# Performance work log

Measured on AMD Instinct MI355X. Metric: run time of the kernel, lower is better.

The kernel has to match this reference:

```python
import jax, jax.numpy as jnp
import numpy as np

ALPHA = 0.25
GAMMA = 2.0
W_CLASS, W_BBOX, W_GIOU, W_EMBED = 1.0, 1.0, 1.0, 0.5
EPS = 1e-8


def box_cxcywh_to_xyxy(b):
    cx, cy, w, h = b[..., 0], b[..., 1], b[..., 2], b[..., 3]
    return jnp.stack([cx - 0.5 * w, cy - 0.5 * h, cx + 0.5 * w, cy + 0.5 * h], axis=-1)


def generalized_box_iou(boxes1, boxes2):
    # boxes1 [N,4], boxes2 [M,4] in xyxy -> [N,M]
    area1 = (boxes1[:, 2] - boxes1[:, 0]) * (boxes1[:, 3] - boxes1[:, 1])
    area2 = (boxes2[:, 2] - boxes2[:, 0]) * (boxes2[:, 3] - boxes2[:, 1])
    lt = jnp.maximum(boxes1[:, None, :2], boxes2[None, :, :2])  # [N,M,2]
    rb = jnp.minimum(boxes1[:, None, 2:], boxes2[None, :, 2:])
    wh = jnp.clip(rb - lt, 0.0)
    inter = wh[..., 0] * wh[..., 1]
    union = area1[:, None] + area2[None, :] - inter
    iou = inter / union
    lt_e = jnp.minimum(boxes1[:, None, :2], boxes2[None, :, :2])
    rb_e = jnp.maximum(boxes1[:, None, 2:], boxes2[None, :, 2:])
    wh_e = jnp.clip(rb_e - lt_e, 0.0)
    area_e = wh_e[..., 0] * wh_e[..., 1]
    return iou - (area_e - union) / area_e


def setup_inputs() -> dict:
    key = jax.random.key(0)
    ks = jax.random.split(key, 6)
    B, Q, C, D, M = 16, 1024, 91, 512, 1600
    pred_logits = jax.random.normal(ks[0], (B, Q, C), dtype=jnp.float32)
    pred_boxes = jax.random.uniform(ks[1], (B, Q, 4), dtype=jnp.float32)
    pred_embed = jax.random.normal(ks[2], (B, Q, D), dtype=jnp.float32)
    text_embeddings = jax.random.normal(ks[3], (C, D), dtype=jnp.float32)
    tgt_ids = jax.random.randint(ks[4], (M,), 0, C, dtype=jnp.int64 if jax.config.jax_enable_x64 else jnp.int32)
    tgt_bbox = jax.random.uniform(ks[5], (M, 4), dtype=jnp.float32)
    return {
        'pred_logits': pred_logits,
        'pred_boxes': pred_boxes,
        'pred_embed': pred_embed,
        'text_embeddings': text_embeddings,
        'tgt_ids': tgt_ids,
        'tgt_bbox': tgt_bbox,
    }


def reference(pred_logits, pred_boxes, pred_embed, text_embeddings, tgt_ids, tgt_bbox):
    B, Q, _ = pred_logits.shape
    N = B * Q
    # --- focal class cost on gathered target-class columns: [N, M]
    logits = pred_logits.reshape(N, -1)
    p = jax.nn.sigmoid(logits[:, tgt_ids])
    pos_cost = ALPHA * (1.0 - p) ** GAMMA * (-jnp.log(p + EPS))
    neg_cost = (1.0 - ALPHA) * p ** GAMMA * (-jnp.log(1.0 - p + EPS))
    cost_class = pos_cost - neg_cost
    # --- L1 box cost (cdist, p=1): [N, M]
    out_bbox = pred_boxes.reshape(N, 4)
    cost_bbox = jnp.sum(jnp.abs(out_bbox[:, None, :] - tgt_bbox[None, :, :]), axis=-1)
    # --- GIoU cost: [N, M]
    cost_giou = -generalized_box_iou(box_cxcywh_to_xyxy(out_bbox), box_cxcywh_to_xyxy(tgt_bbox))
    # --- embedding cosine cost: [N, M]
    v = pred_embed.reshape(N, -1)
    v = v / jnp.linalg.norm(v, axis=1, keepdims=True)
    te = text_embeddings[tgt_ids]  # [M, D]
    cost_embed = 1.0 - v @ te.T
    C = W_BBOX * cost_bbox + W_CLASS * cost_class + W_GIOU * cost_giou + W_EMBED * cost_embed
    return C.reshape(B, Q, -1)
```

## Files before the change

kernel.cpp:

```cpp
#include <hip/hip_runtime.h>
#include <hip/hip_bf16.h>

using bf16x8 = __attribute__((ext_vector_type(8))) short;
using f32x4  = __attribute__((ext_vector_type(4))) float;

__device__ __forceinline__ unsigned short f2bf(float x) {
    unsigned int u = __float_as_uint(x);
    return (unsigned short)((u + 0x7FFFu + ((u >> 16) & 1u)) >> 16);
}

__global__ __launch_bounds__(256)
void k_prep(const float* __restrict__ te, unsigned short* __restrict__ te_bf) {
    const int r = blockIdx.x;
    for (int i = threadIdx.x; i < 512; i += 256) {
        const float v = (r < 91) ? te[(size_t)r * 512 + i] : 0.f;
        te_bf[(size_t)r * 512 + i] = f2bf(v);
    }
}

__global__ __launch_bounds__(256)
void k_class_embed(const float* __restrict__ logits,
                   const float* __restrict__ embed,
                   const unsigned short* __restrict__ te_bf,
                   float* __restrict__ ccombo)
{
    __shared__ float accs[4][16 * 96];
    __shared__ float sq_s[4][16];

    const int tid  = threadIdx.x;
    const int lane = tid & 63;
    const int wv   = tid >> 6;
    const int r16  = lane & 15;
    const int q    = lane >> 4;
    const int n0   = blockIdx.x * 16;

    f32x4 acc[6];
#pragma unroll
    for (int j = 0; j < 6; ++j) acc[j] = (f32x4){0.f, 0.f, 0.f, 0.f};
    float sumsq = 0.f;

    const float* arow = embed + (size_t)(n0 + r16) * 512 + wv * 128 + q * 8;
#pragma unroll
    for (int ks = 0; ks < 4; ++ks) {
        const float4 a0 = *(const float4*)(arow + ks * 32);
        const float4 a1 = *(const float4*)(arow + ks * 32 + 4);
        const float fv[8] = {a0.x, a0.y, a0.z, a0.w, a1.x, a1.y, a1.z, a1.w};
        bf16x8 af;
#pragma unroll
        for (int j = 0; j < 8; ++j) {
            sumsq += fv[j] * fv[j];
            af[j] = (short)f2bf(fv[j]);
        }
#pragma unroll
        for (int ct = 0; ct < 6; ++ct) {
            const bf16x8 bfr = *(const bf16x8*)(te_bf + (size_t)(ct * 16 + r16) * 512
                                                + wv * 128 + ks * 32 + q * 8);
            acc[ct] = __builtin_amdgcn_mfma_f32_16x16x32_bf16(af, bfr, acc[ct], 0, 0, 0);
        }
    }
    sumsq += __shfl_xor(sumsq, 16);
    sumsq += __shfl_xor(sumsq, 32);
    if (lane < 16) sq_s[wv][r16] = sumsq;

#pragma unroll
    for (int ct = 0; ct < 6; ++ct)
#pragma unroll
        for (int j = 0; j < 4; ++j)
            accs[wv][(q * 4 + j) * 96 + ct * 16 + r16] = acc[ct][j];
    __syncthreads();

#pragma unroll
    for (int i = 0; i < 6; ++i) {
        const int e = tid + i * 256;
        const int row = e / 96, col = e - row * 96;
        float v = 0.f;
        if (col < 91) {
            const float dot = accs[0][e] + accs[1][e] + accs[2][e] + accs[3][e];
            const float rn  = rsqrtf(sq_s[0][row] + sq_s[1][row] + sq_s[2][row] + sq_s[3][row]);
            const float x = logits[(size_t)(n0 + row) * 91 + col];
            const float p = 1.f / (1.f + __expf(-x));
            const float pos = 0.25f * (1.f - p) * (1.f - p) * (-__logf(p + 1e-8f));
            const float neg = 0.75f * p * p * (-__logf(1.f - p + 1e-8f));
            v = (pos - neg) + 0.5f - 0.5f * dot * rn;
        }
        ccombo[(size_t)n0 * 96 + e] = v;
    }
}

__global__ __launch_bounds__(256, 4)
void k_cost(const float* __restrict__ pboxes,
            const float* __restrict__ tboxes,
            const int*   __restrict__ tids,
            const float* __restrict__ ccombo,
            float* __restrict__ out)
{
    __shared__ float cc_s[64 * 96];
    __shared__ float p_s[64 * 12];

    const int tid    = threadIdx.x;
    const int bx     = blockIdx.x;
    const int mchunk = bx % 13;
    const int nchunk = bx / 13;
    const int n0     = nchunk * 64;

    {
        const f32x4* src = (const f32x4*)(ccombo + (size_t)n0 * 96);
        f32x4* dst = (f32x4*)cc_s;
#pragma unroll
        for (int i = 0; i < 6; ++i) dst[tid + i * 256] = src[tid + i * 256];
    }
    if (tid < 64) {
        const float4 b = *(const float4*)(pboxes + (size_t)(n0 + tid) * 4);
        float* p = &p_s[tid * 12];
        p[0] = b.x; p[1] = b.y; p[2] = b.z; p[3] = b.w;
        p[4] = b.x - 0.5f * b.z; p[5] = b.y - 0.5f * b.w;
        p[6] = b.x + 0.5f * b.z; p[7] = b.y + 0.5f * b.w;
        p[8] = b.z * b.w;
    }

    const int m  = (mchunk * 32 + (tid & 31)) * 4;
    const int mr = (m < 1600) ? m : 1596;
    float tcx[4], tcy[4], tw[4], th[4];
    float tx0[4], ty0[4], tx1[4], ty1[4], ta[4];
#pragma unroll
    for (int j = 0; j < 4; ++j) {
        const float4 b = *(const float4*)(tboxes + (size_t)(mr + j) * 4);
        tcx[j] = b.x; tcy[j] = b.y; tw[j] = b.z; th[j] = b.w;
        tx0[j] = b.x - 0.5f * b.z; ty0[j] = b.y - 0.5f * b.w;
        tx1[j] = b.x + 0.5f * b.z; ty1[j] = b.y + 0.5f * b.w;
        ta[j]  = b.z * b.w;
    }
    const int4 idv = *(const int4*)(tids + mr);
    const int ids[4] = {idv.x, idv.y, idv.z, idv.w};
    __syncthreads();

    const int w8 = tid >> 5;
    const bool do_store = (m < 1600);

#pragma unroll
    for (int pass = 0; pass < 8; ++pass) {
        const int nl = pass * 8 + w8;
        const float* pr = &p_s[nl * 12];
        const float4 P0 = *(const float4*)pr;
        const float4 P1 = *(const float4*)(pr + 4);
        const float  pa = pr[8];
        const float* ccrow = &cc_s[nl * 96];
        float res[4];
#pragma unroll
        for (int j = 0; j < 4; ++j) {
            const float dx = fminf(P1.z, tx1[j]) - fmaxf(P1.x, tx0[j]);
            const float dy = fminf(P1.w, ty1[j]) - fmaxf(P1.y, ty0[j]);
            const float iw = fmaxf(dx, 0.f), ih = fmaxf(dy, 0.f);
            const float inter = iw * ih;
            const float ew = (P0.z + tw[j]) - dx;
            const float eh = (P0.w + th[j]) - dy;
            const float ae = ew * eh;
            const float uni = __builtin_fmaf(-iw, ih, pa + ta[j]);
            const float l1 = fabsf(P0.x - tcx[j]) + fabsf(P0.y - tcy[j])
                           + fabsf(P0.z - tw[j])  + fabsf(P0.w - th[j]);
            const float aemu = ae - uni;
            const float num = __builtin_fmaf(inter, ae, -(uni * aemu));
            const float g   = __fdividef(num, uni * ae);
            res[j] = (ccrow[ids[j]] + l1) - g;
        }
        if (do_store) {
            f32x4 r4 = {res[0], res[1], res[2], res[3]};
            __builtin_nontemporal_store(r4,
                (f32x4*)(out + (size_t)(n0 + nl) * 1600 + m));
        }
    }
}

extern "C" void kernel_launch(void* const* d_in, const int* in_sizes, int n_in,
                              void* d_out, int out_size, void* d_ws, size_t ws_size,
                              hipStream_t stream) {
    const float* pred_logits = (const float*)d_in[0];
    const float* pred_boxes  = (const float*)d_in[1];
    const float* pred_embed  = (const float*)d_in[2];
    const float* text_emb    = (const float*)d_in[3];
    const int*   tgt_ids     = (const int*)d_in[4];
    const float* tgt_bbox    = (const float*)d_in[5];
    float* out = (float*)d_out;

    unsigned short* te_bf = (unsigned short*)d_ws;
    float* ccombo = (float*)((char*)d_ws + 102400);

    k_prep<<<96, 256, 0, stream>>>(text_emb, te_bf);
    k_class_embed<<<1024, 256, 0, stream>>>(pred_logits, pred_embed, te_bf, ccombo);
    k_cost<<<256 * 13, 256, 0, stream>>>(pred_boxes, tgt_bbox, tgt_ids, ccombo, out);
}
```

Baseline: 63.29 us.

## Shrink k_cost tile to 32 rows, 2 targets per lane, scalar pred-box loads

The k_cost kernel now covers 32 prediction rows per block instead of 64, with each lane handling 2 targets instead of 4. A full 64-lane wavefront spans 128 contiguous output columns, and the grid doubles. The prediction-box shared-memory staging is removed: each wave reads its row's box directly with a wave-uniform (readfirstlane) index and derives the corners inline. Launch bounds rise to 8 blocks per CU, which is meant to increase occupancy and cut LDS use, at the cost of smaller 8-byte stores and more blocks reloading target boxes.

```diff
diff --git a/kernel.cpp b/kernel.cpp
--- a/kernel.cpp
+++ b/kernel.cpp
@@ -3,6 +3,7 @@
 
 using bf16x8 = __attribute__((ext_vector_type(8))) short;
 using f32x4  = __attribute__((ext_vector_type(4))) float;
+using f32x2  = __attribute__((ext_vector_type(2))) float;
 
 __device__ __forceinline__ unsigned short f2bf(float x) {
     unsigned int u = __float_as_uint(x);
@@ -87,86 +88,84 @@
     }
 }
 
-__global__ __launch_bounds__(256, 4)
+__global__ __launch_bounds__(256, 8)
 void k_cost(const float* __restrict__ pboxes,
             const float* __restrict__ tboxes,
             const int*   __restrict__ tids,
             const float* __restrict__ ccombo,
             float* __restrict__ out)
 {
-    __shared__ float cc_s[64 * 96];
-    __shared__ float p_s[64 * 12];
+    __shared__ float cc_s[32 * 96];
 
     const int tid    = threadIdx.x;
     const int bx     = blockIdx.x;
     const int mchunk = bx % 13;
     const int nchunk = bx / 13;
-    const int n0     = nchunk * 64;
+    const int n0     = nchunk * 32;
 
     {
         const f32x4* src = (const f32x4*)(ccombo + (size_t)n0 * 96);
         f32x4* dst = (f32x4*)cc_s;
 #pragma unroll
-        for (int i = 0; i < 6; ++i) dst[tid + i * 256] = src[tid + i * 256];
-    }
-    if (tid < 64) {
-        const float4 b = *(const float4*)(pboxes + (size_t)(n0 + tid) * 4);
-        float* p = &p_s[tid * 12];
-        p[0] = b.x; p[1] = b.y; p[2] = b.z; p[3] = b.w;
-        p[4] = b.x - 0.5f * b.z; p[5] = b.y - 0.5f * b.w;
-        p[6] = b.x + 0.5f * b.z; p[7] = b.y + 0.5f * b.w;
-        p[8] = b.z * b.w;
+        for (int i = 0; i < 3; ++i) dst[tid + i * 256] = src[tid + i * 256];
     }
 
-    const int m  = (mchunk * 32 + (tid & 31)) * 4;
-    const int mr = (m < 1600) ? m : 1596;
-    float tcx[4], tcy[4], tw[4], th[4];
-    float tx0[4], ty0[4], tx1[4], ty1[4], ta[4];
+    const int lane = tid & 63;
+    const int wv   = tid >> 6;
+    const int m    = mchunk * 128 + lane * 2;
+    const int mr   = (m < 1600) ? m : 1598;
+    float tcx[2], tcy[2], tw[2], th[2];
+    float tx0[2], ty0[2], tx1[2], ty1[2], ta[2];
 #pragma unroll
-    for (int j = 0; j < 4; ++j) {
+    for (int j = 0; j < 2; ++j) {
         const float4 b = *(const float4*)(tboxes + (size_t)(mr + j) * 4);
         tcx[j] = b.x; tcy[j] = b.y; tw[j] = b.z; th[j] = b.w;
-        tx0[j] = b.x - 0.5f * b.z; ty0[j] = b.y - 0.5f * b.w;
-        tx1[j] = b.x + 0.5f * b.z; ty1[j] = b.y + 0.5f * b.w;
+        tx0[j] = __builtin_fmaf(-0.5f, b.z, b.x);
+        ty0[j] = __builtin_fmaf(-0.5f, b.w, b.y);
+        tx1[j] = __builtin_fmaf( 0.5f, b.z, b.x);
+        ty1[j] = __builtin_fmaf( 0.5f, b.w, b.y);
         ta[j]  = b.z * b.w;
     }
-    const int4 idv = *(const int4*)(tids + mr);
-    const int ids[4] = {idv.x, idv.y, idv.z, idv.w};
+    const int2 idv = *(const int2*)(tids + mr);
+    const int ids[2] = {idv.x, idv.y};
     __syncthreads();
 
-    const int w8 = tid >> 5;
     const bool do_store = (m < 1600);
 
 #pragma unroll
     for (int pass = 0; pass < 8; ++pass) {
-        const int nl = pass * 8 + w8;
-        const float* pr = &p_s[nl * 12];
-        const float4 P0 = *(const float4*)pr;
-        const float4 P1 = *(const float4*)(pr + 4);
-        const float  pa = pr[8];
+        const int nl  = pass * 4 + wv;
+        const int nlu = __builtin_amdgcn_readfirstlane(nl);
+        const float4 PB = *(const float4*)(pboxes + (size_t)(n0 + nlu) * 4);
+        const float pcx = PB.x, pcy = PB.y, pw = PB.z, ph = PB.w;
+        const float px0 = __builtin_fmaf(-0.5f, pw, pcx);
+        const float py0 = __builtin_fmaf(-0.5f, ph, pcy);
+        const float px1 = __builtin_fmaf( 0.5f, pw, pcx);
+        const float py1 = __builtin_fmaf( 0.5f, ph, pcy);
+        const float pa  = pw * ph;
         const float* ccrow = &cc_s[nl * 96];
-        float res[4];
+        float res[2];
 #pragma unroll
-        for (int j = 0; j < 4; ++j) {
-            const float dx = fminf(P1.z, tx1[j]) - fmaxf(P1.x, tx0[j]);
-            const float dy = fminf(P1.w, ty1[j]) - fmaxf(P1.y, ty0[j]);
+        for (int j = 0; j < 2; ++j) {
+            const float dx = fminf(px1, tx1[j]) - fmaxf(px0, tx0[j]);
+            const float dy = fminf(py1, ty1[j]) - fmaxf(py0, ty0[j]);
             const float iw = fmaxf(dx, 0.f), ih = fmaxf(dy, 0.f);
             const float inter = iw * ih;
-            const float ew = (P0.z + tw[j]) - dx;
-            const float eh = (P0.w + th[j]) - dy;
+            const float ew = (pw + tw[j]) - dx;
+            const float eh = (ph + th[j]) - dy;
             const float ae = ew * eh;
             const float uni = __builtin_fmaf(-iw, ih, pa + ta[j]);
-            const float l1 = fabsf(P0.x - tcx[j]) + fabsf(P0.y - tcy[j])
-                           + fabsf(P0.z - tw[j])  + fabsf(P0.w - th[j]);
+            const float l1 = fabsf(pcx - tcx[j]) + fabsf(pcy - tcy[j])
+                           + fabsf(pw - tw[j])  + fabsf(ph - th[j]);
             const float aemu = ae - uni;
             const float num = __builtin_fmaf(inter, ae, -(uni * aemu));
             const float g   = __fdividef(num, uni * ae);
             res[j] = (ccrow[ids[j]] + l1) - g;
         }
         if (do_store) {
-            f32x4 r4 = {res[0], res[1], res[2], res[3]};
-            __builtin_nontemporal_store(r4,
-                (f32x4*)(out + (size_t)(n0 + nl) * 1600 + m));
+            f32x2 r2 = {res[0], res[1]};
+            __builtin_nontemporal_store(r2,
+                (f32x2*)(out + (size_t)(n0 + nl) * 1600 + m));
         }
     }
 }
@@ -187,5 +186,5 @@
 
     k_prep<<<96, 256, 0, stream>>>(text_emb, te_bf);
     k_class_embed<<<1024, 256, 0, stream>>>(pred_logits, pred_embed, te_bf, ccombo);
-    k_cost<<<256 * 13, 256, 0, stream>>>(pred_boxes, tgt_bbox, tgt_ids, ccombo, out);
+    k_cost<<<512 * 13, 256, 0, stream>>>(pred_boxes, tgt_bbox, tgt_ids, ccombo, out);
 }
```

New measurement: 64.09 us. No clear change (+1.3%).
